# Performance work log

Measured on AMD Instinct MI355X. Metric: run time of the kernel, lower is better.

## Reference

```python
import jax, jax.numpy as jnp
import numpy as np

DIM = 512  # num_rbf_centers // order, order == 4


def setup_inputs() -> dict:
    key = jax.random.key(0)
    ks = jax.random.split(key, 7)
    std = 0.1
    return {
        "X": jax.random.normal(ks[0], (4096, 32), dtype=jnp.float32),
        "centres": jax.random.normal(ks[1], (2048, 32), dtype=jnp.float32),
        "log_sigmas": jnp.zeros((2048,), dtype=jnp.float32),
        "G0": std * jax.random.normal(ks[2], (512, 64), dtype=jnp.float32),
        "G1": std * jax.random.normal(ks[3], (64, 512, 64), dtype=jnp.float32),
        "G2": std * jax.random.normal(ks[4], (64, 512, 64), dtype=jnp.float32),
        "G3": std * jax.random.normal(ks[5], (64, 512, 32), dtype=jnp.float32),
    }


def _rbf(X, centres, log_sigmas):
    # Euclidean distance via GEMM expansion (same math as (x-c)^2 sum, sqrt)
    sq = (jnp.sum(X * X, axis=1, keepdims=True)
          + jnp.sum(centres * centres, axis=1)[None, :]
          - 2.0 * (X @ centres.T))  # [B, n_centres]
    dist = jnp.sqrt(jnp.maximum(sq, 0.0)) / jnp.exp(log_sigmas)[None, :]
    return jnp.exp(-(dist * dist))  # gaussian basis


def reference(X, centres, log_sigmas, G0, G1, G2, G3):
    phi = _rbf(X, centres, log_sigmas)  # [B, 4*DIM]
    Phi0 = phi[:, 0:DIM]
    Phi1 = phi[:, DIM:2 * DIM]
    Phi2 = phi[:, 2 * DIM:3 * DIM]
    Phi3 = phi[:, 3 * DIM:4 * DIM]
    R0 = jnp.einsum('di,bd->bi', G0, Phi0)        # [B, r]
    R1 = jnp.einsum('idj,bd->ibj', G1, Phi1)      # [r, B, r]
    R2 = jnp.einsum('idj,bd->ibj', G2, Phi2)      # [r, B, r]
    R3 = jnp.einsum('jdl,bd->jbl', G3, Phi3)      # [r, B, out]
    # chained per-sample contraction: bi,ibj,jbk,kbl -> bl
    t1 = jnp.einsum('bi,ibj->bj', R0, R1)
    t2 = jnp.einsum('bj,jbk->bk', t1, R2)
    return jnp.einsum('bk,kbl->bl', t2, R3)
```

## Files before the change

kernel.cpp:

```cpp
#include <hip/hip_runtime.h>
#include <math.h>

#define NB    4096
#define NCEN  2048
#define DX    32
#define SEG   512
#define RK    64
#define CAP   64
#define NBCAP (NB * CAP)
#define NCH   64
#define CHUNK 64
#define QMAX  (NBCAP / CHUNK + SEG)

typedef unsigned short us8 __attribute__((ext_vector_type(8)));
typedef short bfrag __attribute__((ext_vector_type(8)));
typedef float f32x4 __attribute__((ext_vector_type(4)));

static __device__ __forceinline__ int wave_sum_i(int v) {
    v += __shfl_xor(v, 1);  v += __shfl_xor(v, 2);  v += __shfl_xor(v, 4);
    v += __shfl_xor(v, 8);  v += __shfl_xor(v, 16); v += __shfl_xor(v, 32);
    return v;
}
static __device__ __forceinline__ float wave_min_f(float v) {
    v = fminf(v, __shfl_xor(v, 1));  v = fminf(v, __shfl_xor(v, 2));
    v = fminf(v, __shfl_xor(v, 4));  v = fminf(v, __shfl_xor(v, 8));
    v = fminf(v, __shfl_xor(v, 16)); v = fminf(v, __shfl_xor(v, 32));
    return v;
}
static __device__ __forceinline__ unsigned short f2bf(float f) {
    unsigned u = __float_as_uint(f);
    u += 0x7FFFu + ((u >> 16) & 1u);
    return (unsigned short)(u >> 16);
}
static __device__ __forceinline__ float bf2f(unsigned short h) {
    return __uint_as_float(((unsigned)h) << 16);
}

__global__ __launch_bounds__(256) void e_gemm(
    const float* __restrict__ X, const float* __restrict__ C,
    const float* __restrict__ LS, float* __restrict__ E, int* __restrict__ HIST2)
{
    __shared__ float XT[32 * 68];
    __shared__ float CT[32 * 68];
    __shared__ float xn[64];
    __shared__ float2 cni[64];

    const int tid = threadIdx.x;
    const int d0 = blockIdx.x * 64, b0 = blockIdx.y * 64;

    if (blockIdx.y == 0) {
        #pragma unroll
        for (int p = 0; p < 16; ++p)
            HIST2[blockIdx.x * 4096 + p * 256 + tid] = 0;
    }

    #pragma unroll
    for (int p = 0; p < 2; ++p) {
        int f = p * 256 + tid;
        int r = f >> 3, c4 = (f & 7) * 4;
        float4 xv = *(const float4*)&X[(size_t)(b0 + r) * DX + c4];
        XT[(c4 + 0) * 68 + r] = xv.x; XT[(c4 + 1) * 68 + r] = xv.y;
        XT[(c4 + 2) * 68 + r] = xv.z; XT[(c4 + 3) * 68 + r] = xv.w;
        float4 cv = *(const float4*)&C[(size_t)(d0 + r) * DX + c4];
        CT[(c4 + 0) * 68 + r] = cv.x; CT[(c4 + 1) * 68 + r] = cv.y;
        CT[(c4 + 2) * 68 + r] = cv.z; CT[(c4 + 3) * 68 + r] = cv.w;
    }
    __syncthreads();

    if (tid < 64) {
        float s = 0.f;
        for (int k = 0; k < 32; ++k) { float v = XT[k * 68 + tid]; s += v * v; }
        xn[tid] = s;
    } else if (tid < 128) {
        int d = tid - 64;
        float s = 0.f;
        for (int k = 0; k < 32; ++k) { float v = CT[k * 68 + d]; s += v * v; }
        cni[d] = make_float2(s, expf(-2.f * LS[d0 + d]));
    }
    __syncthreads();

    const int ty = tid >> 4, tx = tid & 15;
    float acc[4][4] = {};
    #pragma unroll 8
    for (int k = 0; k < 32; ++k) {
        float4 xv = *(const float4*)&XT[k * 68 + ty * 4];
        float4 cv = *(const float4*)&CT[k * 68 + tx * 4];
        acc[0][0] += xv.x * cv.x; acc[0][1] += xv.x * cv.y;
        acc[0][2] += xv.x * cv.z; acc[0][3] += xv.x * cv.w;
        acc[1][0] += xv.y * cv.x; acc[1][1] += xv.y * cv.y;
        acc[1][2] += xv.y * cv.z; acc[1][3] += xv.y * cv.w;
        acc[2][0] += xv.z * cv.x; acc[2][1] += xv.z * cv.y;
        acc[2][2] += xv.z * cv.z; acc[2][3] += xv.z * cv.w;
        acc[3][0] += xv.w * cv.x; acc[3][1] += xv.w * cv.y;
        acc[3][2] += xv.w * cv.z; acc[3][3] += xv.w * cv.w;
    }

    float2 c0v = cni[tx * 4 + 0], c1v = cni[tx * 4 + 1];
    float2 c2v = cni[tx * 4 + 2], c3v = cni[tx * 4 + 3];
    #pragma unroll
    for (int i = 0; i < 4; ++i) {
        float xb = xn[ty * 4 + i];
        float4 ev;
        ev.x = fmaxf(xb + c0v.x - 2.f * acc[i][0], 0.f) * c0v.y;
        ev.y = fmaxf(xb + c1v.x - 2.f * acc[i][1], 0.f) * c1v.y;
        ev.z = fmaxf(xb + c2v.x - 2.f * acc[i][2], 0.f) * c2v.y;
        ev.w = fmaxf(xb + c3v.x - 2.f * acc[i][3], 0.f) * c3v.y;
        *(float4*)&E[(size_t)(b0 + ty * 4 + i) * NCEN + d0 + tx * 4] = ev;
    }
}

__global__ __launch_bounds__(256) void rowselect(
    const float* __restrict__ E, const float* __restrict__ G0,
    int* __restrict__ CNT, int* __restrict__ IDX, float* __restrict__ VAL,
    int* __restrict__ HIST2, float* __restrict__ R0v)
{
    __shared__ int   sd[CAP];
    __shared__ float sv[CAP];
    __shared__ int   scnt;
    __shared__ float4 red[4][16];

    const int tid = threadIdx.x;
    const int lane = tid & 63;
    const int row = blockIdx.x * 4 + (tid >> 6);
    const int b = blockIdx.x, seg = row & 3;
    const float* er = &E[(size_t)b * NCEN + seg * SEG];

    float4 ea = *(const float4*)&er[lane * 8];
    float4 eb = *(const float4*)&er[lane * 8 + 4];
    float e[8] = {ea.x, ea.y, ea.z, ea.w, eb.x, eb.y, eb.z, eb.w};

    float m = e[0];
    #pragma unroll
    for (int q = 1; q < 8; ++q) m = fminf(m, e[q]);
    m = wave_min_f(m);

    int c0 = 0;
    #pragma unroll
    for (int q = 0; q < 8; ++q) c0 += (e[q] <= m + 9.0f) ? 1 : 0;
    c0 = wave_sum_i(c0);

    float Tp = 9.0f;
    if (c0 > CAP) {
        const float rungs[5] = {7.5f, 6.f, 4.5f, 3.f, 1.5f};
        Tp = 0.75f;
        for (int rI = 0; rI < 5; ++rI) {
            int cc = 0;
            #pragma unroll
            for (int q = 0; q < 8; ++q) cc += (e[q] <= m + rungs[rI]) ? 1 : 0;
            cc = wave_sum_i(cc);
            if (cc <= CAP) { Tp = rungs[rI]; break; }
        }
    }
    const float thr = m + Tp;

    int loc = 0;
    #pragma unroll
    for (int q = 0; q < 8; ++q) loc += (e[q] <= thr) ? 1 : 0;
    int incl = loc, t;
    t = __shfl_up(incl, 1);  if (lane >= 1)  incl += t;
    t = __shfl_up(incl, 2);  if (lane >= 2)  incl += t;
    t = __shfl_up(incl, 4);  if (lane >= 4)  incl += t;
    t = __shfl_up(incl, 8);  if (lane >= 8)  incl += t;
    t = __shfl_up(incl, 16); if (lane >= 16) incl += t;
    t = __shfl_up(incl, 32); if (lane >= 32) incl += t;
    const int excl = incl - loc;
    const int total = __shfl(incl, 63);

    const int base = row * CAP;
    int* h2 = &HIST2[(seg * NCH + (b >> 6)) * SEG];
    int slot = excl;
    #pragma unroll
    for (int q = 0; q < 8; ++q) {
        bool pass = (e[q] <= thr);
        if (pass && slot < CAP) {
            if (seg == 0) {
                sd[slot] = lane * 8 + q;
                sv[slot] = expf(-e[q]);
            } else {
                IDX[base + slot] = lane * 8 + q;
                VAL[base + slot] = expf(-e[q]);
                atomicAdd(&h2[lane * 8 + q], 1);
            }
        }
        if (pass) slot++;
    }
    if (lane == 0) CNT[row] = total < CAP ? total : CAP;
    if (seg == 0 && lane == 0) scnt = total < CAP ? total : CAP;
    __syncthreads();

    const int wv = tid >> 6;
    const int tg = lane >> 4, iq = lane & 15;
    const int cnt0 = scnt;
    float4 acc = make_float4(0.f, 0.f, 0.f, 0.f);
    for (int tt = wv * 4 + tg; tt < cnt0; tt += 16) {
        int d = sd[tt];
        float v = sv[tt];
        float4 g = *(const float4*)&G0[(size_t)d * RK + iq * 4];
        acc.x += v * g.x; acc.y += v * g.y; acc.z += v * g.z; acc.w += v * g.w;
    }
    acc.x += __shfl_xor(acc.x, 16); acc.y += __shfl_xor(acc.y, 16);
    acc.z += __shfl_xor(acc.z, 16); acc.w += __shfl_xor(acc.w, 16);
    acc.x += __shfl_xor(acc.x, 32); acc.y += __shfl_xor(acc.y, 32);
    acc.z += __shfl_xor(acc.z, 32); acc.w += __shfl_xor(acc.w, 32);
    if (lane < 16) red[wv][iq] = acc;
    __syncthreads();
    if (tid < 16) {
        float4 a0 = red[0][tid], a1 = red[1][tid];
        float4 a2 = red[2][tid], a3 = red[3][tid];
        float4 s4;
        s4.x = (a0.x + a1.x) + (a2.x + a3.x);
        s4.y = (a0.y + a1.y) + (a2.y + a3.y);
        s4.z = (a0.z + a1.z) + (a2.z + a3.z);
        s4.w = (a0.w + a1.w) + (a2.w + a3.w);
        *(float4*)&R0v[(size_t)b * RK + tid * 4] = s4;
    }
}

__global__ __launch_bounds__(256) void scan2_kernel(
    const int* __restrict__ HIST2, int* __restrict__ OFFS,
    int* __restrict__ LEN, int* __restrict__ CHOFF,
    int* __restrict__ Q, int* __restrict__ QCNT)
{
    __shared__ int wsum[4], wsum2[4];
    const int seg = blockIdx.x;
    const int tid = threadIdx.x;
    const int lane = tid & 63, wave = tid >> 6;
    const int d0 = tid * 2, d1 = tid * 2 + 1;

    int tot0 = 0, tot1 = 0;
    for (int c = 0; c < NCH; ++c) {
        tot0 += HIST2[(seg * NCH + c) * SEG + d0];
        tot1 += HIST2[(seg * NCH + c) * SEG + d1];
    }
    int s = tot0 + tot1;
    int incl = s, t;
    t = __shfl_up(incl, 1);  if (lane >= 1)  incl += t;
    t = __shfl_up(incl, 2);  if (lane >= 2)  incl += t;
    t = __shfl_up(incl, 4);  if (lane >= 4)  incl += t;
    t = __shfl_up(incl, 8);  if (lane >= 8)  incl += t;
    t = __shfl_up(incl, 16); if (lane >= 16) incl += t;
    t = __shfl_up(incl, 32); if (lane >= 32) incl += t;
    if (lane == 63) wsum[wave] = incl;
    const int nch0 = (tot0 + CHUNK - 1) / CHUNK, nch1 = (tot1 + CHUNK - 1) / CHUNK;
    int s2 = nch0 + nch1;
    int incl2 = s2;
    t = __shfl_up(incl2, 1);  if (lane >= 1)  incl2 += t;
    t = __shfl_up(incl2, 2);  if (lane >= 2)  incl2 += t;
    t = __shfl_up(incl2, 4);  if (lane >= 4)  incl2 += t;
    t = __shfl_up(incl2, 8);  if (lane >= 8)  incl2 += t;
    t = __shfl_up(incl2, 16); if (lane >= 16) incl2 += t;
    t = __shfl_up(incl2, 32); if (lane >= 32) incl2 += t;
    if (lane == 63) wsum2[wave] = incl2;
    __syncthreads();
    int woff = 0, woff2 = 0;
    #pragma unroll
    for (int w = 0; w < 4; ++w) if (w < wave) { woff += wsum[w]; woff2 += wsum2[w]; }
    const int excl  = woff + incl - s;
    const int excl2 = woff2 + incl2 - s2;

    OFFS[seg * SEG + d0] = excl;
    OFFS[seg * SEG + d1] = excl + tot0;
    LEN[seg * SEG + d0] = tot0;
    LEN[seg * SEG + d1] = tot1;

    int run0 = excl, run1 = excl + tot0;
    for (int c = 0; c < NCH; ++c) {
        int i0 = (seg * NCH + c) * SEG + d0;
        CHOFF[i0] = run0;     run0 += HIST2[i0];
        CHOFF[i0 + 1] = run1; run1 += HIST2[i0 + 1];
    }

    int qb = excl2;
    for (int c = 0; c < nch0; ++c) Q[seg * QMAX + qb + c] = (d0 << 16) | c;
    qb += nch0;
    for (int c = 0; c < nch1; ++c) Q[seg * QMAX + qb + c] = (d1 << 16) | c;
    if (tid == 255) QCNT[seg] = woff2 + incl2;
}

__global__ __launch_bounds__(256) void scatter_kernel(
    const int* __restrict__ CNT, const int* __restrict__ IDX,
    const float* __restrict__ VAL, const int* __restrict__ CHOFF,
    int* __restrict__ BL, float* __restrict__ PV, int* __restrict__ FWD)
{
    __shared__ int cur[SEG];
    const int tid = threadIdx.x;
    const int chunk = blockIdx.x;
    const int seg = blockIdx.y + 1;
    cur[tid] = CHOFF[(seg * NCH + chunk) * SEG + tid];
    cur[tid + 256] = CHOFF[(seg * NCH + chunk) * SEG + tid + 256];
    __syncthreads();

    const int wave = tid >> 6, lane = tid & 63;
    #pragma unroll 4
    for (int i = 0; i < 16; ++i) {
        const int b = chunk * 64 + wave * 16 + i;
        const int cnt = CNT[b * 4 + seg];
        if (lane < cnt) {
            const int base = (b * 4 + seg) * CAP;
            int d = IDX[base + lane];
            float v = VAL[base + lane];
            int pos = atomicAdd(&cur[d], 1);
            BL[(size_t)(seg - 1) * NBCAP + pos] = b;
            PV[(size_t)(seg - 1) * NBCAP + pos] = v;
            FWD[(size_t)(seg - 1) * NBCAP + pos] = b * CAP + lane;
        }
    }
}

template <int J>
__global__ __launch_bounds__(256) void g_split(
    const float* __restrict__ G, unsigned short* __restrict__ GTH,
    unsigned short* __restrict__ GTL)
{
    __shared__ float g[64][J + 4];
    const int d = blockIdx.x;
    const int tid = threadIdx.x;
    #pragma unroll
    for (int p = 0; p < J / 16; ++p) {
        int id = p * 256 + tid;
        int k = id / (J / 4), j0 = (id % (J / 4)) * 4;
        *(float4*)&g[k][j0] = *(const float4*)&G[((size_t)k * SEG + d) * J + j0];
    }
    __syncthreads();
    constexpr int TPJ = 256 / J;
    constexpr int KPT = 64 / TPJ;
    const int j = tid / TPJ, k0 = (tid % TPJ) * KPT;
    #pragma unroll
    for (int vb = 0; vb < KPT / 8; ++vb) {
        us8 vh, vl;
        #pragma unroll
        for (int e = 0; e < 8; ++e) {
            float x = g[k0 + vb * 8 + e][j];
            unsigned short h = f2bf(x);
            vh[e] = h;
            vl[e] = f2bf(x - bf2f(h));
        }
        *(us8*)&GTH[((size_t)d * J + j) * 64 + k0 + vb * 8] = vh;
        *(us8*)&GTL[((size_t)d * J + j) * 64 + k0 + vb * 8] = vl;
    }
}

template <int NOUT>
__global__ __launch_bounds__(256) void inv_stage_mfma(
    const float* __restrict__ TIN,
    const unsigned short* __restrict__ GTH, const unsigned short* __restrict__ GTL,
    const int* __restrict__ Qs, const int* __restrict__ QCNTs,
    const int* __restrict__ LENs, const int* __restrict__ OFFSs,
    const int* __restrict__ BLs, const float* __restrict__ PVs,
    const int* __restrict__ FWDs, unsigned short* __restrict__ CONTRIB)
{
    constexpr int KP  = 88;
    constexpr int KPo = 80;
    __shared__ alignas(16) unsigned short tinH[64 * KP];
    __shared__ alignas(16) unsigned short tinL[64 * KP];
    __shared__ alignas(16) unsigned short gH[NOUT * KP];
    __shared__ alignas(16) unsigned short gL[NOUT * KP];
    __shared__ float ph[64];
    __shared__ int   fw[64];

    if ((int)blockIdx.x >= QCNTs[0]) return;
    const int tid = threadIdx.x;
    const int desc = Qs[blockIdx.x];
    const int d = desc >> 16, cidx = desc & 0xffff;
    const int len = LENs[d];
    const int off0 = OFFSs[d];
    const int ebase = cidx * CHUNK;

    {
        const unsigned short* sH = &GTH[(size_t)d * (NOUT * 64)];
        const unsigned short* sL = &GTL[(size_t)d * (NOUT * 64)];
        #pragma unroll
        for (int p = 0; p < NOUT / 32; ++p) {
            int id = p * 256 + tid;
            int j = id >> 3, k0 = (id & 7) * 8;
            *(us8*)&gH[j * KP + k0] = *(const us8*)&sH[id * 8];
            *(us8*)&gL[j * KP + k0] = *(const us8*)&sL[id * 8];
        }
    }
    #pragma unroll
    for (int p = 0; p < 4; ++p) {
        int f = p * 256 + tid;
        int en = f >> 4, c4 = (f & 15) * 4;
        int eidx = ebase + en;
        int brow = (eidx < len) ? BLs[off0 + eidx] : 0;
        float4 tv = *(const float4*)&TIN[(size_t)brow * RK + c4];
        ushort4 h, l;
        h.x = f2bf(tv.x); l.x = f2bf(tv.x - bf2f(h.x));
        h.y = f2bf(tv.y); l.y = f2bf(tv.y - bf2f(h.y));
        h.z = f2bf(tv.z); l.z = f2bf(tv.z - bf2f(h.z));
        h.w = f2bf(tv.w); l.w = f2bf(tv.w - bf2f(h.w));
        *(ushort4*)&tinH[en * KP + c4] = h;
        *(ushort4*)&tinL[en * KP + c4] = l;
    }
    if (tid < 64) {
        int ie = ebase + tid;
        bool ok = ie < len;
        ph[tid] = ok ? PVs[off0 + ie] : 0.f;
        fw[tid] = ok ? FWDs[off0 + ie] : 0;
    }
    __syncthreads();

    const int lane = tid & 63;
    const int wv = tid >> 6;
    const int arow = ((wv << 4) | (lane & 15)) * KP;
    const int kg = (lane >> 4) << 3;
    const bfrag aH0 = *(const bfrag*)&tinH[arow + kg];
    const bfrag aH1 = *(const bfrag*)&tinH[arow + 32 + kg];
    const bfrag aL0 = *(const bfrag*)&tinL[arow + kg];
    const bfrag aL1 = *(const bfrag*)&tinL[arow + 32 + kg];

    constexpr int NT = NOUT / 16;
    f32x4 acc[NT];
    #pragma unroll
    for (int jt = 0; jt < NT; ++jt) {
        acc[jt] = (f32x4)(0.0f);
        const int brow = (jt * 16 + (lane & 15)) * KP;
        bfrag bH0 = *(const bfrag*)&gH[brow + kg];
        bfrag bL0 = *(const bfrag*)&gL[brow + kg];
        bfrag bH1 = *(const bfrag*)&gH[brow + 32 + kg];
        bfrag bL1 = *(const bfrag*)&gL[brow + 32 + kg];
        acc[jt] = __builtin_amdgcn_mfma_f32_16x16x32_bf16(aH0, bH0, acc[jt], 0, 0, 0);
        acc[jt] = __builtin_amdgcn_mfma_f32_16x16x32_bf16(aL0, bH0, acc[jt], 0, 0, 0);
        acc[jt] = __builtin_amdgcn_mfma_f32_16x16x32_bf16(aH0, bL0, acc[jt], 0, 0, 0);
        acc[jt] = __builtin_amdgcn_mfma_f32_16x16x32_bf16(aH1, bH1, acc[jt], 0, 0, 0);
        acc[jt] = __builtin_amdgcn_mfma_f32_16x16x32_bf16(aL1, bH1, acc[jt], 0, 0, 0);
        acc[jt] = __builtin_amdgcn_mfma_f32_16x16x32_bf16(aH1, bL1, acc[jt], 0, 0, 0);
    }

    __syncthreads();
    unsigned short* sout = tinH;
    {
        const int r0 = (wv << 4) | ((lane >> 4) << 2);
        const int col = lane & 15;
        const float p0 = ph[r0 + 0], p1 = ph[r0 + 1];
        const float p2 = ph[r0 + 2], p3 = ph[r0 + 3];
        #pragma unroll
        for (int jt = 0; jt < NT; ++jt) {
            sout[(r0 + 0) * KPo + jt * 16 + col] = f2bf(acc[jt][0] * p0);
            sout[(r0 + 1) * KPo + jt * 16 + col] = f2bf(acc[jt][1] * p1);
            sout[(r0 + 2) * KPo + jt * 16 + col] = f2bf(acc[jt][2] * p2);
            sout[(r0 + 3) * KPo + jt * 16 + col] = f2bf(acc[jt][3] * p3);
        }
    }
    __syncthreads();

    constexpr int VPT = NOUT / 32;
    #pragma unroll
    for (int v = 0; v < VPT; ++v) {
        int id = v * 256 + tid;
        int en = id / (NOUT / 8);
        int jp = (id % (NOUT / 8)) * 8;
        if (ebase + en < len) {
            int dst = fw[en];
            us8 val = *(const us8*)&sout[en * KPo + jp];
            *(us8*)&CONTRIB[(size_t)dst * NOUT + jp] = val;
        }
    }
}

template <int NOUT, int EPT>
__global__ __launch_bounds__(256) void inv_stage(
    const float* __restrict__ TIN, const float* __restrict__ G,
    const int* __restrict__ Qs, const int* __restrict__ QCNTs,
    const int* __restrict__ LENs, const int* __restrict__ OFFSs,
    const int* __restrict__ BLs, const float* __restrict__ PVs,
    const int* __restrict__ FWDs, unsigned short* __restrict__ CONTRIB)
{
    constexpr int JL = NOUT / 4;
    constexpr int NG = 256 / JL;
    constexpr int CH = NG * EPT;
    static_assert(CH == CHUNK, "chunk mismatch");
    __shared__ float gd[64 * NOUT];
    __shared__ float tins[CH * 68];

    if ((int)blockIdx.x >= QCNTs[0]) return;
    const int tid = threadIdx.x;
    const int desc = Qs[blockIdx.x];
    const int d = desc >> 16, cidx = desc & 0xffff;
    const int len = LENs[d];
    const int off0 = OFFSs[d];
    const int ebase = cidx * CH;

    #pragma unroll
    for (int p = 0; p < (64 * NOUT / 4) / 256; ++p) {
        int f = p * 256 + tid;
        int k = f / (NOUT / 4), jj = f % (NOUT / 4);
        *(float4*)&gd[k * NOUT + jj * 4] =
            *(const float4*)&G[((size_t)k * SEG + d) * NOUT + jj * 4];
    }
    #pragma unroll
    for (int p = 0; p < 4; ++p) {
        int f = p * 256 + tid;
        int en = f >> 4, c4 = (f & 15) * 4;
        int eidx = ebase + en;
        int brow = (eidx < len) ? BLs[off0 + eidx] : 0;
        *(float4*)&tins[en * 68 + c4] =
            *(const float4*)&TIN[(size_t)brow * RK + c4];
    }
    __syncthreads();

    const int egp = tid / JL, jq = tid % JL;
    float4 a[EPT];
    #pragma unroll
    for (int q = 0; q < EPT; ++q) a[q] = make_float4(0.f, 0.f, 0.f, 0.f);

    #pragma unroll 4
    for (int kq = 0; kq < 16; ++kq) {
        float4 tv[EPT];
        #pragma unroll
        for (int q = 0; q < EPT; ++q)
            tv[q] = *(const float4*)&tins[(egp * EPT + q) * 68 + kq * 4];
        #pragma unroll
        for (int kk = 0; kk < 4; ++kk) {
            float4 gv = *(const float4*)&gd[(kq * 4 + kk) * NOUT + jq * 4];
            #pragma unroll
            for (int q = 0; q < EPT; ++q) {
                float tvk = (kk == 0) ? tv[q].x : (kk == 1) ? tv[q].y
                          : (kk == 2) ? tv[q].z : tv[q].w;
                a[q].x += tvk * gv.x; a[q].y += tvk * gv.y;
                a[q].z += tvk * gv.z; a[q].w += tvk * gv.w;
            }
        }
    }
    #pragma unroll
    for (int q = 0; q < EPT; ++q) {
        const int ie = ebase + egp * EPT + q;
        if (ie < len) {
            float ph = PVs[off0 + ie];
            int dst = FWDs[off0 + ie];
            ushort4 v;
            v.x = f2bf(ph * a[q].x); v.y = f2bf(ph * a[q].y);
            v.z = f2bf(ph * a[q].z); v.w = f2bf(ph * a[q].w);
            *(ushort4*)&CONTRIB[(size_t)dst * NOUT + jq * 4] = v;
        }
    }
}

template <int NOUT>
__global__ __launch_bounds__(256) void gather_kernel(
    const int* __restrict__ CNT, const unsigned short* __restrict__ CONTRIB,
    float* __restrict__ TOUT, int seg)
{
    constexpr int JL = NOUT / 4;
    constexpr int TG = 64 / JL;
    const int tid = threadIdx.x;
    const int b = blockIdx.x * 4 + (tid >> 6);
    const int lane = tid & 63;
    const int tg = lane / JL, iq = lane % JL;
    const int cnt = CNT[b * 4 + seg];
    const unsigned short* src = &CONTRIB[(size_t)b * CAP * NOUT];
    float4 acc = make_float4(0.f, 0.f, 0.f, 0.f);
    #pragma unroll 2
    for (int t = tg; t < cnt; t += TG) {
        ushort4 v = *(const ushort4*)&src[(size_t)t * NOUT + iq * 4];
        acc.x += bf2f(v.x); acc.y += bf2f(v.y);
        acc.z += bf2f(v.z); acc.w += bf2f(v.w);
    }
    #pragma unroll
    for (int off = JL; off < 64; off <<= 1) {
        acc.x += __shfl_xor(acc.x, off); acc.y += __shfl_xor(acc.y, off);
        acc.z += __shfl_xor(acc.z, off); acc.w += __shfl_xor(acc.w, off);
    }
    if (tg == 0) *(float4*)&TOUT[(size_t)b * NOUT + iq * 4] = acc;
}

extern "C" void kernel_launch(void* const* d_in, const int* in_sizes, int n_in,
                              void* d_out, int out_size, void* d_ws, size_t ws_size,
                              hipStream_t stream)
{
    const float* X  = (const float*)d_in[0];
    const float* C  = (const float*)d_in[1];
    const float* LS = (const float*)d_in[2];
    const float* G0 = (const float*)d_in[3];
    const float* G1 = (const float*)d_in[4];
    const float* G2 = (const float*)d_in[5];
    const float* G3 = (const float*)d_in[6];
    float* out = (float*)d_out;

    char* ws = (char*)d_ws;
    float*          E       = (float*)ws;
    unsigned short* CONTRIB = (unsigned short*)ws;
    size_t o = (size_t)NB * NCEN * 4;
    int*   CNT   = (int*)(ws + o);   o += (size_t)NB * 4 * 4;
    int*   IDX   = (int*)(ws + o);   o += (size_t)NB * 4 * CAP * 4;
    float* VAL   = (float*)(ws + o); o += (size_t)NB * 4 * CAP * 4;
    int*   FWD   = (int*)(ws + o);   o += (size_t)3 * NBCAP * 4;
    int*   HIST2 = (int*)(ws + o);   o += (size_t)4 * NCH * SEG * 4;
    int*   CHOFF = (int*)(ws + o);   o += (size_t)4 * NCH * SEG * 4;
    int*   OFFS  = (int*)(ws + o);   o += 4 * SEG * 4;
    int*   LEN   = (int*)(ws + o);   o += 4 * SEG * 4;
    int*   Q     = (int*)(ws + o);   o += (size_t)4 * QMAX * 4;
    int*   QCNT  = (int*)(ws + o);   o += 64;
    int*   BL    = (int*)(ws + o);   o += (size_t)3 * NBCAP * 4;
    float* PV    = (float*)(ws + o); o += (size_t)3 * NBCAP * 4;
    float* R0v   = (float*)(ws + o); o += (size_t)NB * RK * 4;
    float* t1    = (float*)(ws + o); o += (size_t)NB * RK * 4;
    float* t2    = (float*)(ws + o); o += (size_t)NB * RK * 4;

    unsigned short* GTH = (unsigned short*)IDX;
    unsigned short* GTL = (unsigned short*)VAL;

    e_gemm<<<dim3(NCEN / 64, NB / 64), 256, 0, stream>>>(X, C, LS, E, HIST2);
    rowselect<<<NB, 256, 0, stream>>>(E, G0, CNT, IDX, VAL, HIST2, R0v);
    scan2_kernel<<<4, 256, 0, stream>>>(HIST2, OFFS, LEN, CHOFF, Q, QCNT);
    scatter_kernel<<<dim3(NCH, 3), 256, 0, stream>>>(CNT, IDX, VAL, CHOFF, BL, PV, FWD);

    g_split<64><<<SEG, 256, 0, stream>>>(G1, GTH, GTL);
    inv_stage_mfma<64><<<QMAX, 256, 0, stream>>>(
        R0v, GTH, GTL, Q + 1 * QMAX, QCNT + 1, LEN + SEG, OFFS + SEG,
        BL, PV, FWD, CONTRIB);
    gather_kernel<64><<<NB / 4, 256, 0, stream>>>(CNT, CONTRIB, t1, 1);

    g_split<64><<<SEG, 256, 0, stream>>>(G2, GTH, GTL);
    inv_stage_mfma<64><<<QMAX, 256, 0, stream>>>(
        t1, GTH, GTL, Q + 2 * QMAX, QCNT + 2, LEN + 2 * SEG, OFFS + 2 * SEG,
        BL + (size_t)NBCAP, PV + (size_t)NBCAP, FWD + (size_t)NBCAP, CONTRIB);
    gather_kernel<64><<<NB / 4, 256, 0, stream>>>(CNT, CONTRIB, t2, 2);

    g_split<32><<<SEG, 256, 0, stream>>>(G3, GTH, GTL);
    inv_stage_mfma<32><<<QMAX, 256, 0, stream>>>(
        t2, GTH, GTL, Q + 3 * QMAX, QCNT + 3, LEN + 3 * SEG, OFFS + 3 * SEG,
        BL + (size_t)2 * NBCAP, PV + (size_t)2 * NBCAP, FWD + (size_t)2 * NBCAP, CONTRIB);
    gather_kernel<32><<<NB / 4, 256, 0, stream>>>(CNT, CONTRIB, out, 3);
}
```

Baseline: 183.8 us.

## Fold G-split into scan/gather kernels and load swizzled G tiles via async LDS copy

Removes the three standalone g_split launches by appending their blocks to the scan kernel and to the gather kernels of the previous stage, so each weight split overlaps with other work. G tiles are now written pre-swizzled with hi/lo halves in one contiguous buffer, which lets inv_stage_mfma stage them into LDS with global_load_lds async copies and read them through an XOR swizzle instead of padded rows. The scan kernel uses int2 vector loads and stores, and the unused scalar inv_stage kernel is deleted. This adds a separate GT1 workspace buffer and relies on correct buffer aliasing (GT3 reuses GT1, GT2 reuses IDX) across stages.

```diff
diff --git a/kernel.cpp b/kernel.cpp
--- a/kernel.cpp
+++ b/kernel.cpp
@@ -34,6 +34,11 @@
 }
 static __device__ __forceinline__ float bf2f(unsigned short h) {
     return __uint_as_float(((unsigned)h) << 16);
+}
+static __device__ __forceinline__ void async_copy16(const void* g, void* l) {
+    __builtin_amdgcn_global_load_lds(
+        (const __attribute__((address_space(1))) unsigned int*)g,
+        (__attribute__((address_space(3))) unsigned int*)l, 16, 0, 0);
 }
 
 __global__ __launch_bounds__(256) void e_gemm(
@@ -216,21 +221,63 @@
     }
 }
 
-__global__ __launch_bounds__(256) void scan2_kernel(
+template <int J>
+static __device__ __forceinline__ void g_split_dev(
+    const float* __restrict__ G, unsigned short* __restrict__ GT,
+    int d, int tid, char* smem)
+{
+    float (*g)[J + 4] = (float (*)[J + 4])smem;
+    #pragma unroll
+    for (int p = 0; p < J / 16; ++p) {
+        int id = p * 256 + tid;
+        int k = id / (J / 4), j0 = (id % (J / 4)) * 4;
+        *(float4*)&g[k][j0] = *(const float4*)&G[((size_t)k * SEG + d) * J + j0];
+    }
+    __syncthreads();
+    constexpr int TPJ = 256 / J;
+    constexpr int KPT = 64 / TPJ;
+    const int j = tid / TPJ, kc0 = (tid % TPJ) * (KPT / 8);
+    unsigned short* tile = GT + (size_t)d * (2 * J * 64);
+    #pragma unroll
+    for (int vb = 0; vb < KPT / 8; ++vb) {
+        int kchunk = kc0 + vb, k0 = kchunk * 8;
+        us8 vh, vl;
+        #pragma unroll
+        for (int e = 0; e < 8; ++e) {
+            float x = g[k0 + e][j];
+            unsigned short h = f2bf(x);
+            vh[e] = h;
+            vl[e] = f2bf(x - bf2f(h));
+        }
+        int kcs = kchunk ^ (j & 7);
+        *(us8*)&tile[j * 64 + kcs * 8]           = vh;
+        *(us8*)&tile[J * 64 + j * 64 + kcs * 8]  = vl;
+    }
+}
+
+__global__ __launch_bounds__(256) void scan2_split_kernel(
     const int* __restrict__ HIST2, int* __restrict__ OFFS,
     int* __restrict__ LEN, int* __restrict__ CHOFF,
-    int* __restrict__ Q, int* __restrict__ QCNT)
-{
+    int* __restrict__ Q, int* __restrict__ QCNT,
+    const float* __restrict__ G1, unsigned short* __restrict__ GT1)
+{
+    __shared__ alignas(16) char smem[64 * 68 * 4];
     __shared__ int wsum[4], wsum2[4];
+
+    if ((int)blockIdx.x >= 4) {
+        g_split_dev<64>(G1, GT1, (int)blockIdx.x - 4, threadIdx.x, smem);
+        return;
+    }
+
     const int seg = blockIdx.x;
     const int tid = threadIdx.x;
     const int lane = tid & 63, wave = tid >> 6;
-    const int d0 = tid * 2, d1 = tid * 2 + 1;
+    const int d0 = tid * 2;
 
     int tot0 = 0, tot1 = 0;
     for (int c = 0; c < NCH; ++c) {
-        tot0 += HIST2[(seg * NCH + c) * SEG + d0];
-        tot1 += HIST2[(seg * NCH + c) * SEG + d1];
+        int2 h = *(const int2*)&HIST2[(seg * NCH + c) * SEG + d0];
+        tot0 += h.x; tot1 += h.y;
     }
     int s = tot0 + tot1;
     int incl = s, t;
@@ -259,21 +306,22 @@
     const int excl2 = woff2 + incl2 - s2;
 
     OFFS[seg * SEG + d0] = excl;
-    OFFS[seg * SEG + d1] = excl + tot0;
+    OFFS[seg * SEG + d0 + 1] = excl + tot0;
     LEN[seg * SEG + d0] = tot0;
-    LEN[seg * SEG + d1] = tot1;
+    LEN[seg * SEG + d0 + 1] = tot1;
 
     int run0 = excl, run1 = excl + tot0;
     for (int c = 0; c < NCH; ++c) {
         int i0 = (seg * NCH + c) * SEG + d0;
-        CHOFF[i0] = run0;     run0 += HIST2[i0];
-        CHOFF[i0 + 1] = run1; run1 += HIST2[i0 + 1];
+        int2 h = *(const int2*)&HIST2[i0];
+        *(int2*)&CHOFF[i0] = make_int2(run0, run1);
+        run0 += h.x; run1 += h.y;
     }
 
     int qb = excl2;
     for (int c = 0; c < nch0; ++c) Q[seg * QMAX + qb + c] = (d0 << 16) | c;
     qb += nch0;
-    for (int c = 0; c < nch1; ++c) Q[seg * QMAX + qb + c] = (d1 << 16) | c;
+    for (int c = 0; c < nch1; ++c) Q[seg * QMAX + qb + c] = ((d0 + 1) << 16) | c;
     if (tid == 255) QCNT[seg] = woff2 + incl2;
 }
 
@@ -307,74 +355,38 @@
     }
 }
 
-template <int J>
-__global__ __launch_bounds__(256) void g_split(
-    const float* __restrict__ G, unsigned short* __restrict__ GTH,
-    unsigned short* __restrict__ GTL)
-{
-    __shared__ float g[64][J + 4];
-    const int d = blockIdx.x;
-    const int tid = threadIdx.x;
-    #pragma unroll
-    for (int p = 0; p < J / 16; ++p) {
-        int id = p * 256 + tid;
-        int k = id / (J / 4), j0 = (id % (J / 4)) * 4;
-        *(float4*)&g[k][j0] = *(const float4*)&G[((size_t)k * SEG + d) * J + j0];
-    }
-    __syncthreads();
-    constexpr int TPJ = 256 / J;
-    constexpr int KPT = 64 / TPJ;
-    const int j = tid / TPJ, k0 = (tid % TPJ) * KPT;
-    #pragma unroll
-    for (int vb = 0; vb < KPT / 8; ++vb) {
-        us8 vh, vl;
-        #pragma unroll
-        for (int e = 0; e < 8; ++e) {
-            float x = g[k0 + vb * 8 + e][j];
-            unsigned short h = f2bf(x);
-            vh[e] = h;
-            vl[e] = f2bf(x - bf2f(h));
-        }
-        *(us8*)&GTH[((size_t)d * J + j) * 64 + k0 + vb * 8] = vh;
-        *(us8*)&GTL[((size_t)d * J + j) * 64 + k0 + vb * 8] = vl;
-    }
-}
-
 template <int NOUT>
 __global__ __launch_bounds__(256) void inv_stage_mfma(
-    const float* __restrict__ TIN,
-    const unsigned short* __restrict__ GTH, const unsigned short* __restrict__ GTL,
+    const float* __restrict__ TIN, const unsigned short* __restrict__ GT,
     const int* __restrict__ Qs, const int* __restrict__ QCNTs,
     const int* __restrict__ LENs, const int* __restrict__ OFFSs,
     const int* __restrict__ BLs, const float* __restrict__ PVs,
     const int* __restrict__ FWDs, unsigned short* __restrict__ CONTRIB)
 {
-    constexpr int KP  = 88;
-    constexpr int KPo = 80;
+    constexpr int KP = 88;
     __shared__ alignas(16) unsigned short tinH[64 * KP];
     __shared__ alignas(16) unsigned short tinL[64 * KP];
-    __shared__ alignas(16) unsigned short gH[NOUT * KP];
-    __shared__ alignas(16) unsigned short gL[NOUT * KP];
+    __shared__ alignas(16) unsigned short gHL[2 * NOUT * 64];
     __shared__ float ph[64];
     __shared__ int   fw[64];
 
     if ((int)blockIdx.x >= QCNTs[0]) return;
     const int tid = threadIdx.x;
+    const int lane = tid & 63;
+    const int wv = tid >> 6;
     const int desc = Qs[blockIdx.x];
     const int d = desc >> 16, cidx = desc & 0xffff;
     const int len = LENs[d];
     const int off0 = OFFSs[d];
     const int ebase = cidx * CHUNK;
 
+    constexpr int NCHK = (2 * NOUT * 64 * 2) / 1024;
     {
-        const unsigned short* sH = &GTH[(size_t)d * (NOUT * 64)];
-        const unsigned short* sL = &GTL[(size_t)d * (NOUT * 64)];
+        const char* gsrc = (const char*)(GT + (size_t)d * (2 * NOUT * 64));
         #pragma unroll
-        for (int p = 0; p < NOUT / 32; ++p) {
-            int id = p * 256 + tid;
-            int j = id >> 3, k0 = (id & 7) * 8;
-            *(us8*)&gH[j * KP + k0] = *(const us8*)&sH[id * 8];
-            *(us8*)&gL[j * KP + k0] = *(const us8*)&sL[id * 8];
+        for (int i = 0; i < NCHK / 4; ++i) {
+            int c = wv * (NCHK / 4) + i;
+            async_copy16(gsrc + c * 1024 + lane * 16, (char*)gHL + c * 1024);
         }
     }
     #pragma unroll
@@ -400,8 +412,6 @@
     }
     __syncthreads();
 
-    const int lane = tid & 63;
-    const int wv = tid >> 6;
     const int arow = ((wv << 4) | (lane & 15)) * KP;
     const int kg = (lane >> 4) << 3;
     const bfrag aH0 = *(const bfrag*)&tinH[arow + kg];
@@ -409,16 +419,20 @@
     const bfrag aL0 = *(const bfrag*)&tinL[arow + kg];
     const bfrag aL1 = *(const bfrag*)&tinL[arow + 32 + kg];
 
+    const int col = lane & 15;
+    const int kc = lane >> 4;
     constexpr int NT = NOUT / 16;
     f32x4 acc[NT];
     #pragma unroll
     for (int jt = 0; jt < NT; ++jt) {
         acc[jt] = (f32x4)(0.0f);
-        const int brow = (jt * 16 + (lane & 15)) * KP;
-        bfrag bH0 = *(const bfrag*)&gH[brow + kg];
-        bfrag bL0 = *(const bfrag*)&gL[brow + kg];
-        bfrag bH1 = *(const bfrag*)&gH[brow + 32 + kg];
-        bfrag bL1 = *(const bfrag*)&gL[brow + 32 + kg];
+        const int jb = jt * 16 + col;
+        const int sw = jb & 7;
+        const int rb = jb * 64;
+        bfrag bH0 = *(const bfrag*)&gHL[rb + ((kc ^ sw) * 8)];
+        bfrag bH1 = *(const bfrag*)&gHL[rb + (((kc + 4) ^ sw) * 8)];
+        bfrag bL0 = *(const bfrag*)&gHL[NOUT * 64 + rb + ((kc ^ sw) * 8)];
+        bfrag bL1 = *(const bfrag*)&gHL[NOUT * 64 + rb + (((kc + 4) ^ sw) * 8)];
         acc[jt] = __builtin_amdgcn_mfma_f32_16x16x32_bf16(aH0, bH0, acc[jt], 0, 0, 0);
         acc[jt] = __builtin_amdgcn_mfma_f32_16x16x32_bf16(aL0, bH0, acc[jt], 0, 0, 0);
         acc[jt] = __builtin_amdgcn_mfma_f32_16x16x32_bf16(aH0, bL0, acc[jt], 0, 0, 0);
@@ -431,15 +445,14 @@
     unsigned short* sout = tinH;
     {
         const int r0 = (wv << 4) | ((lane >> 4) << 2);
-        const int col = lane & 15;
         const float p0 = ph[r0 + 0], p1 = ph[r0 + 1];
         const float p2 = ph[r0 + 2], p3 = ph[r0 + 3];
         #pragma unroll
         for (int jt = 0; jt < NT; ++jt) {
-            sout[(r0 + 0) * KPo + jt * 16 + col] = f2bf(acc[jt][0] * p0);
-            sout[(r0 + 1) * KPo + jt * 16 + col] = f2bf(acc[jt][1] * p1);
-            sout[(r0 + 2) * KPo + jt * 16 + col] = f2bf(acc[jt][2] * p2);
-            sout[(r0 + 3) * KPo + jt * 16 + col] = f2bf(acc[jt][3] * p3);
+            sout[(r0 + 0) * KP + jt * 16 + col] = f2bf(acc[jt][0] * p0);
+            sout[(r0 + 1) * KP + jt * 16 + col] = f2bf(acc[jt][1] * p1);
+            sout[(r0 + 2) * KP + jt * 16 + col] = f2bf(acc[jt][2] * p2);
+            sout[(r0 + 3) * KP + jt * 16 + col] = f2bf(acc[jt][3] * p3);
         }
     }
     __syncthreads();
@@ -452,88 +465,44 @@
         int jp = (id % (NOUT / 8)) * 8;
         if (ebase + en < len) {
             int dst = fw[en];
-            us8 val = *(const us8*)&sout[en * KPo + jp];
+            us8 val = *(const us8*)&sout[en * KP + jp];
             *(us8*)&CONTRIB[(size_t)dst * NOUT + jp] = val;
         }
     }
 }
 
-template <int NOUT, int EPT>
-__global__ __launch_bounds__(256) void inv_stage(
-    const float* __restrict__ TIN, const float* __restrict__ G,
-    const int* __restrict__ Qs, const int* __restrict__ QCNTs,
-    const int* __restrict__ LENs, const int* __restrict__ OFFSs,
-    const int* __restrict__ BLs, const float* __restrict__ PVs,
-    const int* __restrict__ FWDs, unsigned short* __restrict__ CONTRIB)
-{
+template <int NOUT, int JSPLIT>
+__global__ __launch_bounds__(256) void gather_split_kernel(
+    const int* __restrict__ CNT, const unsigned short* __restrict__ CONTRIB,
+    float* __restrict__ TOUT, int seg,
+    const float* __restrict__ Gn, unsigned short* __restrict__ GTn)
+{
+    __shared__ alignas(16) char smem[64 * 68 * 4];
+    if ((int)blockIdx.x >= NB / 4) {
+        g_split_dev<JSPLIT>(Gn, GTn, (int)blockIdx.x - NB / 4, threadIdx.x, smem);
+        return;
+    }
     constexpr int JL = NOUT / 4;
-    constexpr int NG = 256 / JL;
-    constexpr int CH = NG * EPT;
-    static_assert(CH == CHUNK, "chunk mismatch");
-    __shared__ float gd[64 * NOUT];
-    __shared__ float tins[CH * 68];
-
-    if ((int)blockIdx.x >= QCNTs[0]) return;
-    const int tid = threadIdx.x;
-    const int desc = Qs[blockIdx.x];
-    const int d = desc >> 16, cidx = desc & 0xffff;
-    const int len = LENs[d];
-    const int off0 = OFFSs[d];
-    const int ebase = cidx * CH;
-
-    #pragma unroll
-    for (int p = 0; p < (64 * NOUT / 4) / 256; ++p) {
-        int f = p * 256 + tid;
-        int k = f / (NOUT / 4), jj = f % (NOUT / 4);
-        *(float4*)&gd[k * NOUT + jj * 4] =
-            *(const float4*)&G[((size_t)k * SEG + d) * NOUT + jj * 4];
-    }
-    #pragma unroll
-    for (int p = 0; p < 4; ++p) {
-        int f = p * 256 + tid;
-        int en = f >> 4, c4 = (f & 15) * 4;
-        int eidx = ebase + en;
-        int brow = (eidx < len) ? BLs[off0 + eidx] : 0;
-        *(float4*)&tins[en * 68 + c4] =
-            *(const float4*)&TIN[(size_t)brow * RK + c4];
-    }
-    __syncthreads();
-
-    const int egp = tid / JL, jq = tid % JL;
-    float4 a[EPT];
-    #pragma unroll
-    for (int q = 0; q < EPT; ++q) a[q] = make_float4(0.f, 0.f, 0.f, 0.f);
-
-    #pragma unroll 4
-    for (int kq = 0; kq < 16; ++kq) {
-        float4 tv[EPT];
-        #pragma unroll
-        for (int q = 0; q < EPT; ++q)
-            tv[q] = *(const float4*)&tins[(egp * EPT + q) * 68 + kq * 4];
-        #pragma unroll
-        for (int kk = 0; kk < 4; ++kk) {
-            float4 gv = *(const float4*)&gd[(kq * 4 + kk) * NOUT + jq * 4];
-            #pragma unroll
-            for (int q = 0; q < EPT; ++q) {
-                float tvk = (kk == 0) ? tv[q].x : (kk == 1) ? tv[q].y
-                          : (kk == 2) ? tv[q].z : tv[q].w;
-                a[q].x += tvk * gv.x; a[q].y += tvk * gv.y;
-                a[q].z += tvk * gv.z; a[q].w += tvk * gv.w;
-            }
-        }
-    }
-    #pragma unroll
-    for (int q = 0; q < EPT; ++q) {
-        const int ie = ebase + egp * EPT + q;
-        if (ie < len) {
-            float ph = PVs[off0 + ie];
-            int dst = FWDs[off0 + ie];
-            ushort4 v;
-            v.x = f2bf(ph * a[q].x); v.y = f2bf(ph * a[q].y);
-            v.z = f2bf(ph * a[q].z); v.w = f2bf(ph * a[q].w);
-            *(ushort4*)&CONTRIB[(size_t)dst * NOUT + jq * 4] = v;
-        }
-    }
+    constexpr int TG = 64 / JL;
+    const int tid = threadIdx.x;
+    const int b = blockIdx.x * 4 + (tid >> 6);
+    const int lane = tid & 63;
+    const int tg = lane / JL, iq = lane % JL;
+    const int cnt = CNT[b * 4 + seg];
+    const unsigned short* src = &CONTRIB[(size_t)b * CAP * NOUT];
+    float4 acc = make_float4(0.f, 0.f, 0.f, 0.f);
+    #pragma unroll 2
+    for (int t = tg; t < cnt; t += TG) {
+        ushort4 v = *(const ushort4*)&src[(size_t)t * NOUT + iq * 4];
+        acc.x += bf2f(v.x); acc.y += bf2f(v.y);
+        acc.z += bf2f(v.z); acc.w += bf2f(v.w);
+    }
+    #pragma unroll
+    for (int off = JL; off < 64; off <<= 1) {
+        acc.x += __shfl_xor(acc.x, off); acc.y += __shfl_xor(acc.y, off);
+        acc.z += __shfl_xor(acc.z, off); acc.w += __shfl_xor(acc.w, off);
+    }
+    if (tg == 0) *(float4*)&TOUT[(size_t)b * NOUT + iq * 4] = acc;
 }
 
 template <int NOUT>
@@ -596,30 +565,32 @@
     float* R0v   = (float*)(ws + o); o += (size_t)NB * RK * 4;
     float* t1    = (float*)(ws + o); o += (size_t)NB * RK * 4;
     float* t2    = (float*)(ws + o); o += (size_t)NB * RK * 4;
-
-    unsigned short* GTH = (unsigned short*)IDX;
-    unsigned short* GTL = (unsigned short*)VAL;
+    unsigned short* GT1 = (unsigned short*)(ws + o);
+    o += (size_t)SEG * 2 * 64 * 64 * 2;
+
+    unsigned short* GT2 = (unsigned short*)IDX;
+    unsigned short* GT3 = GT1;
 
     e_gemm<<<dim3(NCEN / 64, NB / 64), 256, 0, stream>>>(X, C, LS, E, HIST2);
     rowselect<<<NB, 256, 0, stream>>>(E, G0, CNT, IDX, VAL, HIST2, R0v);
-    scan2_kernel<<<4, 256, 0, stream>>>(HIST2, OFFS, LEN, CHOFF, Q, QCNT);
+    scan2_split_kernel<<<4 + SEG, 256, 0, stream>>>(
+        HIST2, OFFS, LEN, CHOFF, Q, QCNT, G1, GT1);
     scatter_kernel<<<dim3(NCH, 3), 256, 0, stream>>>(CNT, IDX, VAL, CHOFF, BL, PV, FWD);
 
-    g_split<64><<<SEG, 256, 0, stream>>>(G1, GTH, GTL);
     inv_stage_mfma<64><<<QMAX, 256, 0, stream>>>(
-        R0v, GTH, GTL, Q + 1 * QMAX, QCNT + 1, LEN + SEG, OFFS + SEG,
+        R0v, GT1, Q + 1 * QMAX, QCNT + 1, LEN + SEG, OFFS + SEG,
         BL, PV, FWD, CONTRIB);
-    gather_kernel<64><<<NB / 4, 256, 0, stream>>>(CNT, CONTRIB, t1, 1);
-
-    g_split<64><<<SEG, 256, 0, stream>>>(G2, GTH, GTL);
+    gather_split_kernel<64, 64><<<NB / 4 + SEG, 256, 0, stream>>>(
+        CNT, CONTRIB, t1, 1, G2, GT2);
+
     inv_stage_mfma<64><<<QMAX, 256, 0, stream>>>(
-        t1, GTH, GTL, Q + 2 * QMAX, QCNT + 2, LEN + 2 * SEG, OFFS + 2 * SEG,
+        t1, GT2, Q + 2 * QMAX, QCNT + 2, LEN + 2 * SEG, OFFS + 2 * SEG,
         BL + (size_t)NBCAP, PV + (size_t)NBCAP, FWD + (size_t)NBCAP, CONTRIB);
-    gather_kernel<64><<<NB / 4, 256, 0, stream>>>(CNT, CONTRIB, t2, 2);
-
-    g_split<32><<<SEG, 256, 0, stream>>>(G3, GTH, GTL);
+    gather_split_kernel<64, 32><<<NB / 4 + SEG, 256, 0, stream>>>(
+        CNT, CONTRIB, t2, 2, G3, GT3);
+
     inv_stage_mfma<32><<<QMAX, 256, 0, stream>>>(
-        t2, GTH, GTL, Q + 3 * QMAX, QCNT + 3, LEN + 3 * SEG, OFFS + 3 * SEG,
+        t2, GT3, Q + 3 * QMAX, QCNT + 3, LEN + 3 * SEG, OFFS + 3 * SEG,
         BL + (size_t)2 * NBCAP, PV + (size_t)2 * NBCAP, FWD + (size_t)2 * NBCAP, CONTRIB);
     gather_kernel<32><<<NB / 4, 256, 0, stream>>>(CNT, CONTRIB, out, 3);
 }
```

After: 169.2 us. -7.9%, faster.
